# Kernel tuning notes

Hardware: AMD Instinct MI355X
Metric: run time of the kernel (lower is better)

## Reference

```python
import jax, jax.numpy as jnp
import numpy as np

B, T, N, D = 16, 12, 10000, 2
E = 320000


def setup_inputs() -> dict:
    key = jax.random.key(0)
    k1, k2, k3 = jax.random.split(key, 3)
    predictions = jax.random.normal(k1, (B, T, N, D), dtype=jnp.float32)
    targets = jax.random.normal(k2, (B, T, N, D), dtype=jnp.float32)
    edge_index = jax.random.randint(k3, (2, E), 0, N, dtype=jnp.int64)
    return {"predictions": predictions, "targets": targets, "edge_index": edge_index}


def reference(predictions, targets, edge_index):
    # weights from __init__ defaults
    mse_w, spatial_w, temporal_w, conservation_w = 1.0, 0.1, 0.05, 0.02

    # main loss: MAE (use_mae=True)
    main_loss = jnp.mean(jnp.abs(predictions - targets))

    # spatial consistency: the per-(b,t) python loop of mse over edges,
    # averaged over batch*pred_len, equals one global mean over [B,T,E,D]
    src, dst = edge_index[0], edge_index[1]
    pred_diff = jnp.abs(predictions[:, :, src] - predictions[:, :, dst])  # [B,T,E,D]
    targ_diff = jnp.abs(targets[:, :, src] - targets[:, :, dst])
    spatial_loss = jnp.mean((pred_diff - targ_diff) ** 2)

    # temporal smoothness: first-order time differences
    pd_t = predictions[:, 1:] - predictions[:, :-1]
    td_t = targets[:, 1:] - targets[:, :-1]
    temporal_loss = jnp.mean((pd_t - td_t) ** 2)

    # conservation: sum over nodes
    pred_sum = predictions.sum(axis=2)  # [B,T,D]
    targ_sum = targets.sum(axis=2)
    conservation_loss = jnp.mean((pred_sum - targ_sum) ** 2)

    total_loss = (mse_w * main_loss + spatial_w * spatial_loss
                  + temporal_w * temporal_loss + conservation_w * conservation_loss)

    # order: loss, main_loss, spatial_loss, temporal_loss, conservation_loss
    return jnp.stack([total_loss, main_loss, spatial_loss, temporal_loss, conservation_loss])
```

## Files before the change

kernel.cpp:

```cpp
#include <hip/hip_runtime.h>
#include <hip/hip_fp16.h>

#define BB 16
#define TT 12
#define NN 10000
#define DD 2
#define EE 320000
#define BT 192
#define TOT 3840000
#define SLICE 20000

#define NCH 96
#define SLICES 14
#define EPS 22858
#define SPATB (NCH*SLICES)
#define SPATG (SPATB + BT)

#define PACKB 942
#define EOFFB 1250
#define PREPG (PACKB + EOFFB)

#define EOFF_BOFF 32768
#define W2_BOFF   2623488
#define NEED (W2_BOFF + (size_t)NCH * NN * 2 * 4)

typedef float v2f __attribute__((ext_vector_type(2)));
typedef _Float16 hv2 __attribute__((ext_vector_type(2)));

#if defined(__has_builtin)
#if __has_builtin(__builtin_amdgcn_fdot2)
#define HAVE_FDOT2 1
#endif
#if __has_builtin(__builtin_amdgcn_cvt_scalef32_pk_f16_fp8)
#define HAVE_SCALEF16 1
#endif
#endif

__device__ __forceinline__ __half2 pkh2(float a, float b) {
    auto t = __builtin_amdgcn_cvt_pkrtz(a, b);
    return *reinterpret_cast<__half2*>(&t);
}
__device__ __forceinline__ float dot_acc(__half2 d, float acc) {
#ifdef HAVE_FDOT2
    hv2 dr = *reinterpret_cast<hv2*>(&d);
    return __builtin_amdgcn_fdot2(dr, dr, acc, false);
#else
    float2 f = __half22float2(d);
    return fmaf(f.y, f.y, fmaf(f.x, f.x, acc));
#endif
}
__device__ __forceinline__ void slot_acc(unsigned a, unsigned b, float& acc) {
#ifdef HAVE_SCALEF16
    auto pa = __builtin_amdgcn_cvt_scalef32_pk_f16_fp8(a, 1.0f, false);
    auto ta = __builtin_amdgcn_cvt_scalef32_pk_f16_fp8(a, 1.0f, true);
    auto pb = __builtin_amdgcn_cvt_scalef32_pk_f16_fp8(b, 1.0f, false);
    auto tb = __builtin_amdgcn_cvt_scalef32_pk_f16_fp8(b, 1.0f, true);
    __half2 hpa = *reinterpret_cast<__half2*>(&pa);
    __half2 hta = *reinterpret_cast<__half2*>(&ta);
    __half2 hpb = *reinterpret_cast<__half2*>(&pb);
    __half2 htb = *reinterpret_cast<__half2*>(&tb);
    __half2 d = __hsub2(__habs2(__hsub2(hpa, hpb)), __habs2(__hsub2(hta, htb)));
#else
    v2f ap = __builtin_amdgcn_cvt_pk_f32_fp8((int)a, false);
    v2f at = __builtin_amdgcn_cvt_pk_f32_fp8((int)a, true);
    v2f bp = __builtin_amdgcn_cvt_pk_f32_fp8((int)b, false);
    v2f bq = __builtin_amdgcn_cvt_pk_f32_fp8((int)b, true);
    __half2 d = __hsub2(__habs2(__hsub2(pkh2(ap[0], ap[1]), pkh2(bp[0], bp[1]))),
                        __habs2(__hsub2(pkh2(at[0], at[1]), pkh2(bq[0], bq[1]))));
#endif
    acc = dot_acc(d, acc);
}

__global__ __launch_bounds__(256) void prep_kernel(const float* __restrict__ p,
                                                   const float* __restrict__ tg,
                                                   const int* __restrict__ idx,
                                                   char* __restrict__ wsb) {
    int g = blockIdx.x;
    if (g < PACKB) {
        __shared__ unsigned tile[64][33];
        int ng = g / 6, cg = g % 6;
        int n0 = ng * 64;
        int ln = threadIdx.x & 63, r = threadIdx.x >> 6;
        int n = n0 + ln;
        if (n < NN) {
            for (int sl = r; sl < 32; sl += 4) {
                int bt = cg * 32 + sl;
                size_t e = (size_t)bt * SLICE + (size_t)n * 2;
                float2 pv = *reinterpret_cast<const float2*>(p + e);
                float2 tv = *reinterpret_cast<const float2*>(tg + e);
                int pk = __builtin_amdgcn_cvt_pk_fp8_f32(pv.x, pv.y, 0, false);
                pk = __builtin_amdgcn_cvt_pk_fp8_f32(tv.x, tv.y, pk, true);
                tile[ln][sl] = (unsigned)pk;
            }
        }
        __syncthreads();
        unsigned* w2c = (unsigned*)(wsb + W2_BOFF);
        for (int f = threadIdx.x; f < 2048; f += 256) {
            int c2 = f >> 7, j2 = f & 127;
            int nn2 = j2 >> 1, k2 = j2 & 1;
            int n2 = n0 + nn2;
            if (n2 < NN) {
                int c = cg * 16 + c2;
                w2c[((unsigned)(c * NN + n2) << 1) + k2] = tile[nn2][c2 * 2 + k2];
            }
        }
    } else {
        int e = (g - PACKB) * 256 + threadIdx.x;
        if (e < EE) {
            uint2* eoff = (uint2*)(wsb + EOFF_BOFF);
            eoff[e] = make_uint2((unsigned)idx[e] * 8u,
                                 (unsigned)idx[EE + e] * 8u);
        }
    }
}

__global__ __launch_bounds__(1024, 8) void spatial_kernel(const uint2* __restrict__ w2c2,
                                                          const uint2* __restrict__ eoff,
                                                          const float* __restrict__ p,
                                                          const float* __restrict__ tg,
                                                          float* __restrict__ ws) {
    __shared__ uint2 nd[NN];
    __shared__ float red[64];
    int bid = blockIdx.x;
    int tid = threadIdx.x;

    if (bid < BT) {
        int bt = bid;
        size_t base = (size_t)bt * SLICE;
        bool inner = (bt % TT) < TT - 1;
        const float2* p2  = (const float2*)(p + base);
        const float2* t2  = (const float2*)(tg + base);
        const float2* pn2 = (const float2*)(p + base + SLICE);
        const float2* tn2 = (const float2*)(tg + base + SLICE);
        float m = 0.f, w = 0.f, cx = 0.f, cy = 0.f;
        for (int j = tid; j < NN; j += 1024) {
            float2 pv = p2[j], tv = t2[j];
            m += fabsf(pv.x - tv.x) + fabsf(pv.y - tv.y);
            cx += pv.x - tv.x;
            cy += pv.y - tv.y;
            if (inner) {
                float2 pn = pn2[j], tn = tn2[j];
                float d0 = (pn.x - pv.x) - (tn.x - tv.x);
                float d1 = (pn.y - pv.y) - (tn.y - tv.y);
                w = fmaf(d0, d0, w);
                w = fmaf(d1, d1, w);
            }
        }
        for (int o = 32; o; o >>= 1) {
            m += __shfl_xor(m, o); w += __shfl_xor(w, o);
            cx += __shfl_xor(cx, o); cy += __shfl_xor(cy, o);
        }
        int wid = tid >> 6;
        if ((tid & 63) == 0) {
            red[wid] = m; red[16 + wid] = w; red[32 + wid] = cx; red[48 + wid] = cy;
        }
        __syncthreads();
        if (tid == 0) {
            float M = 0, W = 0, CX = 0, CY = 0;
            for (int k = 0; k < 16; ++k) {
                M += red[k]; W += red[16 + k]; CX += red[32 + k]; CY += red[48 + k];
            }
            ws[bt] = M;
            ws[1536 + bt] = W;
            ws[3072 + 2 * bt] = CX;
            ws[3072 + 2 * bt + 1] = CY;
        }
        return;
    }

    int gb = bid - BT;
    int c = gb % NCH;
    int s = gb / NCH;
    const uint4* src4 = (const uint4*)(w2c2 + (size_t)c * NN);
    uint4* nd4 = (uint4*)nd;
    for (int i = tid; i < NN / 2; i += 1024)
        nd4[i] = src4[i];
    __syncthreads();

    const char* ndb = (const char*)nd;
    int e = s * EPS + tid;
    int eend = (s + 1) * EPS;
    if (eend > EE) eend = EE;
    float acc0 = 0.f, acc1 = 0.f;
    while (e + 1024 < eend) {
        uint2 o1 = eoff[e], o2 = eoff[e + 1024];
        uint2 A1 = *(const uint2*)(ndb + o1.x);
        uint2 B1 = *(const uint2*)(ndb + o1.y);
        uint2 A2 = *(const uint2*)(ndb + o2.x);
        uint2 B2 = *(const uint2*)(ndb + o2.y);
        slot_acc(A1.x, B1.x, acc0);
        slot_acc(A1.y, B1.y, acc1);
        slot_acc(A2.x, B2.x, acc0);
        slot_acc(A2.y, B2.y, acc1);
        e += 2048;
    }
    if (e < eend) {
        uint2 o = eoff[e];
        uint2 A = *(const uint2*)(ndb + o.x);
        uint2 B = *(const uint2*)(ndb + o.y);
        slot_acc(A.x, B.x, acc0);
        slot_acc(A.y, B.y, acc1);
    }
    float acc = acc0 + acc1;
    for (int o = 32; o; o >>= 1) acc += __shfl_xor(acc, o);
    if ((tid & 63) == 0) red[tid >> 6] = acc;
    __syncthreads();
    if (tid == 0) {
        float t = 0.f;
        for (int k = 0; k < 16; ++k) t += red[k];
        ws[6144 + gb] = t;
    }
}

__global__ __launch_bounds__(1024) void finalize_kernel(const float* __restrict__ ws,
                                                        float* __restrict__ out) {
    int tid = threadIdx.x;
    float a = 0, bv = 0, sp = 0, cq = 0;
    if (tid < BT) { a = ws[tid]; bv = ws[1536 + tid]; }
    for (int k = tid; k < SPATB; k += 1024) sp += ws[6144 + k];
    if (tid < BT * DD) { float cs = ws[3072 + tid]; cq = cs * cs; }
    for (int o = 32; o; o >>= 1) {
        a += __shfl_xor(a, o); bv += __shfl_xor(bv, o);
        sp += __shfl_xor(sp, o); cq += __shfl_xor(cq, o);
    }
    __shared__ float ra[16], rb[16], rs[16], rc[16];
    int wid = tid >> 6;
    if ((tid & 63) == 0) { ra[wid] = a; rb[wid] = bv; rs[wid] = sp; rc[wid] = cq; }
    __syncthreads();
    if (tid == 0) {
        float A = 0, B2 = 0, S = 0, C = 0;
        for (int k = 0; k < 16; k++) { A += ra[k]; B2 += rb[k]; S += rs[k]; C += rc[k]; }
        float mainl = A / (float)TOT;
        float temp  = B2 / (float)(BB * (TT - 1) * NN * DD);
        float spat  = S / ((float)BT * (float)EE * (float)DD);
        float cons  = C / (float)(BT * DD);
        out[0] = mainl + 0.1f * spat + 0.05f * temp + 0.02f * cons;
        out[1] = mainl; out[2] = spat; out[3] = temp; out[4] = cons;
    }
}

__global__ __launch_bounds__(256) void stream_fb(const float* __restrict__ p,
                                                 const float* __restrict__ tg,
                                                 float* __restrict__ ws) {
    int b = blockIdx.x;
    int bt = b >> 3, part = b & 7;
    int tt = bt % TT;
    size_t base = (size_t)bt * SLICE;
    bool inner = (tt < TT - 1);
    float m = 0.f, w = 0.f, c = 0.f;
    int j0 = part * 2500;
    for (int j = j0 + threadIdx.x; j < j0 + 2500; j += 256) {
        size_t jj = base + j;
        float pv = p[jj], tv = tg[jj];
        m += fabsf(pv - tv);
        c += pv - tv;
        if (inner) {
            float pn = p[jj + SLICE], tn = tg[jj + SLICE];
            float dd = (pn - pv) - (tn - tv);
            w += dd * dd;
        }
    }
    for (int o = 32; o >= 2; o >>= 1) {
        m += __shfl_xor(m, o); w += __shfl_xor(w, o); c += __shfl_xor(c, o);
    }
    m += __shfl_xor(m, 1);
    w += __shfl_xor(w, 1);
    __shared__ float sm[4], sw[4], s0[4], s1[4];
    int wid = threadIdx.x >> 6, lane = threadIdx.x & 63;
    if (lane == 0) { sm[wid] = m; sw[wid] = w; s0[wid] = c; }
    if (lane == 1) { s1[wid] = c; }
    __syncthreads();
    if (threadIdx.x == 0) {
        float a = 0, bv = 0, c0 = 0, c1 = 0;
        for (int k = 0; k < 4; k++) { a += sm[k]; bv += sw[k]; c0 += s0[k]; c1 += s1[k]; }
        ws[b] = a; ws[1536 + b] = bv;
        ws[3072 + 2 * b] = c0; ws[3072 + 2 * b + 1] = c1;
    }
}

__global__ __launch_bounds__(256) void spatial_fb(const float* __restrict__ p,
                                                  const float* __restrict__ tg,
                                                  const int* __restrict__ idx,
                                                  float* __restrict__ ws) {
    int lane = threadIdx.x & 63;
    int wave = (blockIdx.x * 256 + threadIdx.x) >> 6;
    float s = 0.f;
    for (int e = wave; e < EE; e += SPATB * 4) {
        int sn = idx[e] * DD, dn = idx[EE + e] * DD;
        for (int bt = lane; bt < BT; bt += 64) {
            size_t base = (size_t)bt * SLICE;
            float2 ps = *reinterpret_cast<const float2*>(p + base + sn);
            float2 pd = *reinterpret_cast<const float2*>(p + base + dn);
            float2 ts = *reinterpret_cast<const float2*>(tg + base + sn);
            float2 td = *reinterpret_cast<const float2*>(tg + base + dn);
            float d0 = fabsf(ps.x - pd.x) - fabsf(ts.x - td.x);
            float d1 = fabsf(ps.y - pd.y) - fabsf(ts.y - td.y);
            s = fmaf(d0, d0, s);
            s = fmaf(d1, d1, s);
        }
    }
    for (int o = 32; o; o >>= 1) s += __shfl_xor(s, o);
    __shared__ float sv[4];
    if (lane == 0) sv[threadIdx.x >> 6] = s;
    __syncthreads();
    if (threadIdx.x == 0) ws[6144 + blockIdx.x] = sv[0] + sv[1] + sv[2] + sv[3];
}

__global__ __launch_bounds__(1024) void finalize_fb(const float* __restrict__ ws,
                                                    float* __restrict__ out) {
    int tid = threadIdx.x;
    float a = 0, bv = 0, sp = 0, cq = 0;
    for (int k = tid; k < 1536; k += 1024) { a += ws[k]; bv += ws[1536 + k]; }
    for (int k = tid; k < SPATB; k += 1024) sp += ws[6144 + k];
    if (tid < BT * DD) {
        int bt = tid >> 1, par = tid & 1;
        float cs = 0;
        for (int part = 0; part < 8; ++part)
            cs += ws[3072 + ((bt * 8 + part) << 1) + par];
        cq = cs * cs;
    }
    for (int o = 32; o; o >>= 1) {
        a += __shfl_xor(a, o); bv += __shfl_xor(bv, o);
        sp += __shfl_xor(sp, o); cq += __shfl_xor(cq, o);
    }
    __shared__ float ra[16], rb[16], rs[16], rc[16];
    int wid = tid >> 6;
    if ((tid & 63) == 0) { ra[wid] = a; rb[wid] = bv; rs[wid] = sp; rc[wid] = cq; }
    __syncthreads();
    if (tid == 0) {
        float A = 0, B2 = 0, S = 0, C = 0;
        for (int k = 0; k < 16; k++) { A += ra[k]; B2 += rb[k]; S += rs[k]; C += rc[k]; }
        float mainl = A / (float)TOT;
        float temp  = B2 / (float)(BB * (TT - 1) * NN * DD);
        float spat  = S / ((float)BT * (float)EE * (float)DD);
        float cons  = C / (float)(BT * DD);
        out[0] = mainl + 0.1f * spat + 0.05f * temp + 0.02f * cons;
        out[1] = mainl; out[2] = spat; out[3] = temp; out[4] = cons;
    }
}

extern "C" void kernel_launch(void* const* d_in, const int* in_sizes, int n_in,
                              void* d_out, int out_size, void* d_ws, size_t ws_size,
                              hipStream_t stream) {
    const float* p  = (const float*)d_in[0];
    const float* tg = (const float*)d_in[1];
    const int*   ix = (const int*)d_in[2];
    float* out = (float*)d_out;
    char*  wsb = (char*)d_ws;
    float* ws  = (float*)d_ws;

    if (ws_size >= NEED) {
        prep_kernel<<<PREPG, 256, 0, stream>>>(p, tg, ix, wsb);
        spatial_kernel<<<SPATG, 1024, 0, stream>>>((const uint2*)(wsb + W2_BOFF),
                                                   (const uint2*)(wsb + EOFF_BOFF),
                                                   p, tg, ws);
        finalize_kernel<<<1, 1024, 0, stream>>>(ws, out);
    } else {
        stream_fb<<<1536, 256, 0, stream>>>(p, tg, ws);
        spatial_fb<<<SPATB, 256, 0, stream>>>(p, tg, ix, ws);
        finalize_fb<<<1, 1024, 0, stream>>>(ws, out);
    }
}
```

Before: 48.59 us.

## Fuse finalize into spatial kernel via atomics and last-block reduction

Removes the separate finalize kernel launch. Each block now atomically adds its partial sums into a small accumulator that prep_kernel zeroes, and the last block to finish, detected with an atomic counter, computes the outputs. The streaming part also switches from float2 to float4 loads. The cost is atomic contention on a few addresses and a non-deterministic floating-point summation order. The fallback path grid size is also changed from 1344 to 2048 blocks.

```diff
diff --git a/kernel.cpp b/kernel.cpp
--- a/kernel.cpp
+++ b/kernel.cpp
@@ -20,8 +20,9 @@
 #define EOFFB 1250
 #define PREPG (PACKB + EOFFB)
 
-#define EOFF_BOFF 32768
-#define W2_BOFF   2623488
+#define ACC_F 8192
+#define EOFF_BOFF 65536
+#define W2_BOFF   2656256
 #define NEED (W2_BOFF + (size_t)NCH * NN * 2 * 4)
 
 typedef float v2f __attribute__((ext_vector_type(2)));
@@ -75,6 +76,7 @@
                                                    const float* __restrict__ tg,
                                                    const int* __restrict__ idx,
                                                    char* __restrict__ wsb) {
+    float* ws = (float*)wsb;
     int g = blockIdx.x;
     if (g < PACKB) {
         __shared__ unsigned tile[64][33];
@@ -105,6 +107,8 @@
             }
         }
     } else {
+        if (g == PACKB && threadIdx.x < 16)
+            ws[ACC_F + threadIdx.x] = 0.f;
         int e = (g - PACKB) * 256 + threadIdx.x;
         if (e < EE) {
             uint2* eoff = (uint2*)(wsb + EOFF_BOFF);
@@ -118,32 +122,39 @@
                                                           const uint2* __restrict__ eoff,
                                                           const float* __restrict__ p,
                                                           const float* __restrict__ tg,
-                                                          float* __restrict__ ws) {
+                                                          float* __restrict__ ws,
+                                                          float* __restrict__ out) {
     __shared__ uint2 nd[NN];
     __shared__ float red[64];
     int bid = blockIdx.x;
     int tid = threadIdx.x;
+    float* acc = ws + ACC_F;
 
     if (bid < BT) {
         int bt = bid;
         size_t base = (size_t)bt * SLICE;
         bool inner = (bt % TT) < TT - 1;
-        const float2* p2  = (const float2*)(p + base);
-        const float2* t2  = (const float2*)(tg + base);
-        const float2* pn2 = (const float2*)(p + base + SLICE);
-        const float2* tn2 = (const float2*)(tg + base + SLICE);
+        const float4* p4  = (const float4*)(p + base);
+        const float4* t4  = (const float4*)(tg + base);
+        const float4* pn4 = (const float4*)(p + base + SLICE);
+        const float4* tn4 = (const float4*)(tg + base + SLICE);
         float m = 0.f, w = 0.f, cx = 0.f, cy = 0.f;
-        for (int j = tid; j < NN; j += 1024) {
-            float2 pv = p2[j], tv = t2[j];
-            m += fabsf(pv.x - tv.x) + fabsf(pv.y - tv.y);
-            cx += pv.x - tv.x;
-            cy += pv.y - tv.y;
+        for (int j = tid; j < NN / 2; j += 1024) {
+            float4 pv = p4[j], tv = t4[j];
+            m += fabsf(pv.x - tv.x) + fabsf(pv.y - tv.y)
+               + fabsf(pv.z - tv.z) + fabsf(pv.w - tv.w);
+            cx += (pv.x - tv.x) + (pv.z - tv.z);
+            cy += (pv.y - tv.y) + (pv.w - tv.w);
             if (inner) {
-                float2 pn = pn2[j], tn = tn2[j];
+                float4 pn = pn4[j], tn = tn4[j];
                 float d0 = (pn.x - pv.x) - (tn.x - tv.x);
                 float d1 = (pn.y - pv.y) - (tn.y - tv.y);
+                float d2 = (pn.z - pv.z) - (tn.z - tv.z);
+                float d3 = (pn.w - pv.w) - (tn.w - tv.w);
                 w = fmaf(d0, d0, w);
                 w = fmaf(d1, d1, w);
+                w = fmaf(d2, d2, w);
+                w = fmaf(d3, d3, w);
             }
         }
         for (int o = 32; o; o >>= 1) {
@@ -160,82 +171,71 @@
             for (int k = 0; k < 16; ++k) {
                 M += red[k]; W += red[16 + k]; CX += red[32 + k]; CY += red[48 + k];
             }
-            ws[bt] = M;
-            ws[1536 + bt] = W;
-            ws[3072 + 2 * bt] = CX;
-            ws[3072 + 2 * bt + 1] = CY;
-        }
-        return;
-    }
-
-    int gb = bid - BT;
-    int c = gb % NCH;
-    int s = gb / NCH;
-    const uint4* src4 = (const uint4*)(w2c2 + (size_t)c * NN);
-    uint4* nd4 = (uint4*)nd;
-    for (int i = tid; i < NN / 2; i += 1024)
-        nd4[i] = src4[i];
-    __syncthreads();
-
-    const char* ndb = (const char*)nd;
-    int e = s * EPS + tid;
-    int eend = (s + 1) * EPS;
-    if (eend > EE) eend = EE;
-    float acc0 = 0.f, acc1 = 0.f;
-    while (e + 1024 < eend) {
-        uint2 o1 = eoff[e], o2 = eoff[e + 1024];
-        uint2 A1 = *(const uint2*)(ndb + o1.x);
-        uint2 B1 = *(const uint2*)(ndb + o1.y);
-        uint2 A2 = *(const uint2*)(ndb + o2.x);
-        uint2 B2 = *(const uint2*)(ndb + o2.y);
-        slot_acc(A1.x, B1.x, acc0);
-        slot_acc(A1.y, B1.y, acc1);
-        slot_acc(A2.x, B2.x, acc0);
-        slot_acc(A2.y, B2.y, acc1);
-        e += 2048;
-    }
-    if (e < eend) {
-        uint2 o = eoff[e];
-        uint2 A = *(const uint2*)(ndb + o.x);
-        uint2 B = *(const uint2*)(ndb + o.y);
-        slot_acc(A.x, B.x, acc0);
-        slot_acc(A.y, B.y, acc1);
-    }
-    float acc = acc0 + acc1;
-    for (int o = 32; o; o >>= 1) acc += __shfl_xor(acc, o);
-    if ((tid & 63) == 0) red[tid >> 6] = acc;
-    __syncthreads();
+            atomicAdd(acc + 0, M);
+            atomicAdd(acc + 1, W);
+            atomicAdd(acc + 3, CX * CX + CY * CY);
+        }
+    } else {
+        int gb = bid - BT;
+        int c = gb % NCH;
+        int s = gb / NCH;
+        const uint4* src4 = (const uint4*)(w2c2 + (size_t)c * NN);
+        uint4* nd4 = (uint4*)nd;
+        for (int i = tid; i < NN / 2; i += 1024)
+            nd4[i] = src4[i];
+        __syncthreads();
+
+        const char* ndb = (const char*)nd;
+        int e = s * EPS + tid;
+        int eend = (s + 1) * EPS;
+        if (eend > EE) eend = EE;
+        float acc0 = 0.f, acc1 = 0.f;
+        while (e + 1024 < eend) {
+            uint2 o1 = eoff[e], o2 = eoff[e + 1024];
+            uint2 A1 = *(const uint2*)(ndb + o1.x);
+            uint2 B1 = *(const uint2*)(ndb + o1.y);
+            uint2 A2 = *(const uint2*)(ndb + o2.x);
+            uint2 B2 = *(const uint2*)(ndb + o2.y);
+            slot_acc(A1.x, B1.x, acc0);
+            slot_acc(A1.y, B1.y, acc1);
+            slot_acc(A2.x, B2.x, acc0);
+            slot_acc(A2.y, B2.y, acc1);
+            e += 2048;
+        }
+        if (e < eend) {
+            uint2 o = eoff[e];
+            uint2 A = *(const uint2*)(ndb + o.x);
+            uint2 B = *(const uint2*)(ndb + o.y);
+            slot_acc(A.x, B.x, acc0);
+            slot_acc(A.y, B.y, acc1);
+        }
+        float a = acc0 + acc1;
+        for (int o = 32; o; o >>= 1) a += __shfl_xor(a, o);
+        if ((tid & 63) == 0) red[tid >> 6] = a;
+        __syncthreads();
+        if (tid == 0) {
+            float t = 0.f;
+            for (int k = 0; k < 16; ++k) t += red[k];
+            atomicAdd(acc + 2, t);
+        }
+    }
+
     if (tid == 0) {
-        float t = 0.f;
-        for (int k = 0; k < 16; ++k) t += red[k];
-        ws[6144 + gb] = t;
-    }
-}
-
-__global__ __launch_bounds__(1024) void finalize_kernel(const float* __restrict__ ws,
-                                                        float* __restrict__ out) {
-    int tid = threadIdx.x;
-    float a = 0, bv = 0, sp = 0, cq = 0;
-    if (tid < BT) { a = ws[tid]; bv = ws[1536 + tid]; }
-    for (int k = tid; k < SPATB; k += 1024) sp += ws[6144 + k];
-    if (tid < BT * DD) { float cs = ws[3072 + tid]; cq = cs * cs; }
-    for (int o = 32; o; o >>= 1) {
-        a += __shfl_xor(a, o); bv += __shfl_xor(bv, o);
-        sp += __shfl_xor(sp, o); cq += __shfl_xor(cq, o);
-    }
-    __shared__ float ra[16], rb[16], rs[16], rc[16];
-    int wid = tid >> 6;
-    if ((tid & 63) == 0) { ra[wid] = a; rb[wid] = bv; rs[wid] = sp; rc[wid] = cq; }
-    __syncthreads();
-    if (tid == 0) {
-        float A = 0, B2 = 0, S = 0, C = 0;
-        for (int k = 0; k < 16; k++) { A += ra[k]; B2 += rb[k]; S += rs[k]; C += rc[k]; }
-        float mainl = A / (float)TOT;
-        float temp  = B2 / (float)(BB * (TT - 1) * NN * DD);
-        float spat  = S / ((float)BT * (float)EE * (float)DD);
-        float cons  = C / (float)(BT * DD);
-        out[0] = mainl + 0.1f * spat + 0.05f * temp + 0.02f * cons;
-        out[1] = mainl; out[2] = spat; out[3] = temp; out[4] = cons;
+        __threadfence();
+        unsigned done = atomicAdd((unsigned*)(acc + 4), 1u);
+        if (done == SPATG - 1) {
+            __threadfence();
+            float A  = atomicAdd(acc + 0, 0.f);
+            float B2 = atomicAdd(acc + 1, 0.f);
+            float S  = atomicAdd(acc + 2, 0.f);
+            float C  = atomicAdd(acc + 3, 0.f);
+            float mainl = A / (float)TOT;
+            float temp  = B2 / (float)(BB * (TT - 1) * NN * DD);
+            float spat  = S / ((float)BT * (float)EE * (float)DD);
+            float cons  = C / (float)(BT * DD);
+            out[0] = mainl + 0.1f * spat + 0.05f * temp + 0.02f * cons;
+            out[1] = mainl; out[2] = spat; out[3] = temp; out[4] = cons;
+        }
     }
 }
 
@@ -285,7 +285,7 @@
     int lane = threadIdx.x & 63;
     int wave = (blockIdx.x * 256 + threadIdx.x) >> 6;
     float s = 0.f;
-    for (int e = wave; e < EE; e += SPATB * 4) {
+    for (int e = wave; e < EE; e += 2048 * 4) {
         int sn = idx[e] * DD, dn = idx[EE + e] * DD;
         for (int bt = lane; bt < BT; bt += 64) {
             size_t base = (size_t)bt * SLICE;
@@ -311,7 +311,7 @@
     int tid = threadIdx.x;
     float a = 0, bv = 0, sp = 0, cq = 0;
     for (int k = tid; k < 1536; k += 1024) { a += ws[k]; bv += ws[1536 + k]; }
-    for (int k = tid; k < SPATB; k += 1024) sp += ws[6144 + k];
+    for (int k = tid; k < 2048; k += 1024) sp += ws[6144 + k];
     if (tid < BT * DD) {
         int bt = tid >> 1, par = tid & 1;
         float cs = 0;
@@ -353,11 +353,10 @@
         prep_kernel<<<PREPG, 256, 0, stream>>>(p, tg, ix, wsb);
         spatial_kernel<<<SPATG, 1024, 0, stream>>>((const uint2*)(wsb + W2_BOFF),
                                                    (const uint2*)(wsb + EOFF_BOFF),
-                                                   p, tg, ws);
-        finalize_kernel<<<1, 1024, 0, stream>>>(ws, out);
+                                                   p, tg, ws, out);
     } else {
         stream_fb<<<1536, 256, 0, stream>>>(p, tg, ws);
-        spatial_fb<<<SPATB, 256, 0, stream>>>(p, tg, ix, ws);
+        spatial_fb<<<2048, 256, 0, stream>>>(p, tg, ix, ws);
         finalize_fb<<<1, 1024, 0, stream>>>(ws, out);
     }
 }
```

Result: slower. 81.24 us (+67.2%).
